# Optimization experiments

Hardware: AMD Instinct MI355X
Metric: run time of the kernel (lower is better)

## Reference

```python
import jax, jax.numpy as jnp
import numpy as np

H = 16  # hidden_dim
EPS = 1e-5


def _lstm_layer(x, W_ih, W_hh, b_ih, b_hh):
    # x: [B,T,D_in] -> [B,T,H]; PyTorch gate order i,f,g,o
    B = x.shape[0]
    xg = jnp.einsum('btd,gd->btg', x, W_ih) + (b_ih + b_hh)  # [B,T,4H]

    def step(carry, xt):
        h, c = carry
        gates = xt + h @ W_hh.T
        i, f, g, o = jnp.split(gates, 4, axis=-1)
        c = jax.nn.sigmoid(f) * c + jax.nn.sigmoid(i) * jnp.tanh(g)
        h = jax.nn.sigmoid(o) * jnp.tanh(c)
        return (h, c), h

    h0 = jnp.zeros((B, H), x.dtype)
    _, hs = jax.lax.scan(step, (h0, h0), jnp.swapaxes(xg, 0, 1))  # [T,B,H]
    return jnp.swapaxes(hs, 0, 1)


def setup_inputs() -> dict:
    key = jax.random.key(0)
    ks = jax.random.split(key, 20)
    B, T, D, O = 256, 2048, 57, 4
    x = jax.random.normal(ks[0], (B, T, D), dtype=jnp.float32)
    lengths = jnp.maximum(jnp.sort(jax.random.randint(ks[1], (B,), 1, T + 1))[::-1], 1)
    s = 1.0 / np.sqrt(H)
    u = lambda k, shp: jax.random.uniform(k, shp, jnp.float32, -s, s)
    inp = {'x': x, 'lengths': lengths}
    dims_in = [D, H, H]
    for l in range(3):
        inp[f'W_ih{l}'] = u(ks[2 + 4 * l], (4 * H, dims_in[l]))
        inp[f'W_hh{l}'] = u(ks[3 + 4 * l], (4 * H, H))
        inp[f'b_ih{l}'] = u(ks[4 + 4 * l], (4 * H,))
        inp[f'b_hh{l}'] = u(ks[5 + 4 * l], (4 * H,))
    inp['bn_gamma'] = jnp.ones((H,), jnp.float32)
    inp['bn_beta'] = jnp.zeros((H,), jnp.float32)
    inp['fc_w'] = u(ks[14], (O, H))
    inp['fc_b'] = u(ks[15], (O,))
    return inp


def reference(x, lengths, W_ih0, W_hh0, b_ih0, b_hh0, W_ih1, W_hh1, b_ih1, b_hh1,
              W_ih2, W_hh2, b_ih2, b_hh2, bn_gamma, bn_beta, fc_w, fc_b):
    B, T, _ = x.shape
    h = x
    for W_ih, W_hh, b_ih, b_hh in ((W_ih0, W_hh0, b_ih0, b_hh0),
                                    (W_ih1, W_hh1, b_ih1, b_hh1),
                                    (W_ih2, W_hh2, b_ih2, b_hh2)):
        h = _lstm_layer(h, W_ih, W_hh, b_ih, b_hh)
    # pad_packed_sequence: zero out positions past each sequence length
    mask = (jnp.arange(T)[None, :] < lengths[:, None])[:, :, None].astype(h.dtype)
    h = h * mask  # [B,T,H]
    # BatchNorm1d (training mode) over (batch,time) per channel, incl. padding zeros
    mean = jnp.mean(h, axis=(0, 1))
    var = jnp.mean((h - mean) ** 2, axis=(0, 1))
    norm = (h - mean) * jax.lax.rsqrt(var + EPS) * bn_gamma + bn_beta
    return norm @ fc_w.T + fc_b  # [B,T,4]
```

## Files before the change

kernel.cpp:

```cpp
#include <hip/hip_runtime.h>
#include <math.h>

#define TT 2048
#define BBATCH 256
#define DDIM 57
#define NROWS (BBATCH*TT)
#define NF 524288.0f
#define U 8

#define K1 (-1.4426950408889634f)
#define K2 (-2.8853900817779268f)

__device__ __forceinline__ float bcastl(float v, int k) {
  return __uint_as_float((unsigned)__builtin_amdgcn_readlane((int)__float_as_uint(v), k));
}
__device__ __forceinline__ float rcpf(float x) { return __builtin_amdgcn_rcpf(x); }
__device__ __forceinline__ float exp2f_(float x) { return __builtin_amdgcn_exp2f(x); }

template<int PAT>
__device__ __forceinline__ float quadb(float v) {
  return __int_as_float(__builtin_amdgcn_update_dpp(0, __float_as_int(v), PAT, 0xF, 0xF, true));
}

__global__ void zero_accum_k(float* accum) {
  accum[threadIdx.x] = 0.f;
}

__global__ __launch_bounds__(256) void xg0_gemm_k(
    const float* __restrict__ x, const float* __restrict__ Wih,
    const float* __restrict__ bih, const float* __restrict__ bhh,
    float* __restrict__ xg0)
{
  const int lane = threadIdx.x & 63;
  const int g = (lane & 3) * 16 + (lane >> 2);
  const float fac = ((lane & 3) == 2) ? K2 : K1;
  const int wid  = blockIdx.x * (blockDim.x >> 6) + (threadIdx.x >> 6);
  const int nw   = gridDim.x * (blockDim.x >> 6);
  float w[DDIM];
  #pragma unroll
  for (int d = 0; d < DDIM; ++d) w[d] = fac * Wih[g*DDIM + d];
  const float bias = fac * (bih[g] + bhh[g]);

  int r = wid;
  float xv = 0.f;
  if (r < NROWS && lane < DDIM)
    xv = x[(size_t)__builtin_amdgcn_readfirstlane(r) * DDIM + lane];
  for (; r < NROWS; r += nw) {
    const int rn = r + nw;
    float xn = 0.f;
    if (rn < NROWS && lane < DDIM)
      xn = x[(size_t)__builtin_amdgcn_readfirstlane(rn) * DDIM + lane];
    float a0 = bias, a1 = 0.f, a2 = 0.f, a3 = 0.f;
    #pragma unroll
    for (int d = 0; d < 56; d += 4) {
      a0 += w[d]   * bcastl(xv, d);
      a1 += w[d+1] * bcastl(xv, d+1);
      a2 += w[d+2] * bcastl(xv, d+2);
      a3 += w[d+3] * bcastl(xv, d+3);
    }
    a0 += w[56] * bcastl(xv, 56);
    xg0[(size_t)__builtin_amdgcn_readfirstlane(r) * 64 + lane] = (a0 + a1) + (a2 + a3);
    xv = xn;
  }
}

__global__ __launch_bounds__(192, 1) void lstm_scan_pipe_k(
    const float* __restrict__ xg0,
    const int*   __restrict__ lengths,
    const float* __restrict__ Whh0,
    const float* __restrict__ Wih1, const float* __restrict__ Whh1,
    const float* __restrict__ bih1, const float* __restrict__ bhh1,
    const float* __restrict__ Wih2, const float* __restrict__ Whh2,
    const float* __restrict__ bih2, const float* __restrict__ bhh2,
    float* __restrict__ h2buf, float* __restrict__ accum)
{
  const int tid  = threadIdx.x;
  const int wave = tid >> 6;
  const int lane = tid & 63;
  const int gt   = lane & 3;
  const int ch   = lane >> 2;
  const int g    = gt*16 + ch;
  const int b    = blockIdx.x;
  const int len  = lengths[b];
  const bool isg = (gt == 2);
  const float fac = isg ? K2 : K1;
  const float mg = isg ? 2.f : 1.f;
  const float ag = isg ? -1.f : 0.f;

  __shared__ float lds_h0[2][U][16];
  __shared__ float lds_h1[2][U][16];

  float wa[16], wb[16];
  float bias = 0.f;
  if (wave == 0) {
    #pragma unroll
    for (int k = 0; k < 16; ++k) { wb[k] = fac * Whh0[g*16 + k]; wa[k] = 0.f; }
  } else if (wave == 1) {
    #pragma unroll
    for (int k = 0; k < 16; ++k) { wa[k] = fac * Wih1[g*16 + k]; wb[k] = fac * Whh1[g*16 + k]; }
    bias = fac * (bih1[g] + bhh1[g]);
  } else {
    #pragma unroll
    for (int k = 0; k < 16; ++k) { wa[k] = fac * Wih2[g*16 + k]; wb[k] = fac * Whh2[g*16 + k]; }
    bias = fac * (bih2[g] + bhh2[g]);
  }

  float hs = 0.f, csK = 0.f;
  float sum = 0.f, sq = 0.f;
  const int base = b*TT*64 + lane;
  float* __restrict__ h2row = h2buf + (size_t)b*TT*16;

  auto lstm_update = [&](float dot) {
    float s   = rcpf(1.f + exp2f_(dot));
    float act = fmaf(s, mg, ag);
    float gi = quadb<0x00>(act);
    float gf = quadb<0x55>(act);
    float gg = quadb<0xAA>(act);
    float go = quadb<0xFF>(act);
    csK = fmaf(gf, csK, (K2 * gg) * gi);
    float r = rcpf(1.f + exp2f_(csK));
    hs = go * fmaf(2.f, r, -1.f);
  };
  auto owndot = [&](float seed) {
    float hb[16];
    #pragma unroll
    for (int k = 0; k < 16; ++k) hb[k] = bcastl(hs, 4*k);
    float a0 = seed, a1 = 0.f, a2 = 0.f, a3 = 0.f;
    #pragma unroll
    for (int k = 0; k < 16; k += 4) {
      a0 += wb[k]   * hb[k];
      a1 += wb[k+1] * hb[k+1];
      a2 += wb[k+2] * hb[k+2];
      a3 += wb[k+3] * hb[k+3];
    }
    return (a0 + a1) + (a2 + a3);
  };
  auto indot = [&](const float* hin) {
    float a0 = bias, a1 = 0.f, a2 = 0.f, a3 = 0.f;
    #pragma unroll
    for (int k = 0; k < 16; k += 4) {
      a0 += wa[k]   * hin[k];
      a1 += wa[k+1] * hin[k+1];
      a2 += wa[k+2] * hin[k+2];
      a3 += wa[k+3] * hin[k+3];
    }
    return (a0 + a1) + (a2 + a3);
  };

  const int NS = (len + U - 1) / U;
  const int S  = NS + 2;

  float cur[U], nxt[U];
  if (wave == 0) {
    #pragma unroll
    for (int j = 0; j < U; ++j) cur[j] = xg0[base + j*64];
    #pragma unroll
    for (int j = 0; j < U; ++j) {
      int ip = U + j; ip = ip > TT-1 ? TT-1 : ip;
      nxt[j] = xg0[base + ip*64];
    }
  }

  for (int s = 0; s < S; ++s) {
    const int p = s & 1, q = p ^ 1;
    if (wave == 0) {
      if (s < NS) {
        float ld[U];
        #pragma unroll
        for (int j = 0; j < U; ++j) {
          int ip = (s + 2)*U + j; ip = ip > TT-1 ? TT-1 : ip;
          ld[j] = xg0[base + ip*64];
        }
        #pragma unroll
        for (int j = 0; j < U; ++j) {
          lstm_update(owndot(cur[j]));
          if (gt == 0) lds_h0[p][j][ch] = hs;
        }
        #pragma unroll
        for (int j = 0; j < U; ++j) { cur[j] = nxt[j]; nxt[j] = ld[j]; }
      }
    } else if (wave == 1) {
      if (s >= 1 && s <= NS) {
        float xin[U];
        #pragma unroll
        for (int j = 0; j < U; ++j) {
          const float4* hp = (const float4*)&lds_h0[q][j][0];
          float4 h0v = hp[0], h1v = hp[1], h2v = hp[2], h3v = hp[3];
          float hin[16] = {h0v.x,h0v.y,h0v.z,h0v.w, h1v.x,h1v.y,h1v.z,h1v.w,
                           h2v.x,h2v.y,h2v.z,h2v.w, h3v.x,h3v.y,h3v.z,h3v.w};
          xin[j] = indot(hin);
        }
        #pragma unroll
        for (int j = 0; j < U; ++j) {
          lstm_update(owndot(xin[j]));
          if (gt == 0) lds_h1[p][j][ch] = hs;
        }
      }
    } else {
      if (s >= 2) {
        float xin[U];
        #pragma unroll
        for (int j = 0; j < U; ++j) {
          const float4* hp = (const float4*)&lds_h1[q][j][0];
          float4 h0v = hp[0], h1v = hp[1], h2v = hp[2], h3v = hp[3];
          float hin[16] = {h0v.x,h0v.y,h0v.z,h0v.w, h1v.x,h1v.y,h1v.z,h1v.w,
                           h2v.x,h2v.y,h2v.z,h2v.w, h3v.x,h3v.y,h3v.z,h3v.w};
          xin[j] = indot(hin);
        }
        #pragma unroll
        for (int j = 0; j < U; ++j) {
          lstm_update(owndot(xin[j]));
          const int t = (s - 2)*U + j;
          if (t < len) {
            if (gt == 0) h2row[t*16 + ch] = hs;
            sum += hs; sq += hs*hs;
          }
        }
      }
    }
    __syncthreads();
  }

  for (int idx = len*16 + tid; idx < TT*16; idx += 192)
    h2row[idx] = 0.f;

  if (wave == 2 && gt == 0) {
    atomicAdd(&accum[ch],      sum);
    atomicAdd(&accum[16 + ch], sq);
  }
}

__global__ void prep_k(const float* __restrict__ accum,
                       const float* __restrict__ gamma, const float* __restrict__ beta,
                       const float* __restrict__ fcw, const float* __restrict__ fcb,
                       float* __restrict__ coef)
{
  const int lane = threadIdx.x;
  const int o = lane >> 4, c = lane & 15;
  const float inv_n = 1.0f / NF;
  float mean = accum[c] * inv_n;
  float var  = accum[16 + c] * inv_n - mean*mean;
  float s  = gamma[c] * rsqrtf(var + 1e-5f);
  float tb = beta[c] - mean * s;
  float woc = fcw[o*16 + c];
  coef[lane] = s * woc;
  float term = tb * woc;
  #pragma unroll
  for (int off = 1; off < 16; off <<= 1) term += __shfl_xor(term, off, 16);
  if (c == 0) coef[64 + o] = fcb[o] + term;
}

__global__ __launch_bounds__(256) void finalize_k(
    const float* __restrict__ h2buf, const float* __restrict__ coef,
    float* __restrict__ out)
{
  const int r = blockIdx.x * 256 + threadIdx.x;
  const float4* hp = (const float4*)(h2buf + (size_t)r * 16);
  float4 v0 = hp[0], v1 = hp[1], v2 = hp[2], v3 = hp[3];
  float hv[16] = {v0.x,v0.y,v0.z,v0.w, v1.x,v1.y,v1.z,v1.w,
                  v2.x,v2.y,v2.z,v2.w, v3.x,v3.y,v3.z,v3.w};
  float4 o4;
  float* op = &o4.x;
  #pragma unroll
  for (int o = 0; o < 4; ++o) {
    float a = coef[64 + o];
    #pragma unroll
    for (int c = 0; c < 16; ++c) a += coef[o*16 + c] * hv[c];
    op[o] = a;
  }
  ((float4*)out)[r] = o4;
}

extern "C" void kernel_launch(void* const* d_in, const int* in_sizes, int n_in,
                              void* d_out, int out_size, void* d_ws, size_t ws_size,
                              hipStream_t stream)
{
  const float* x     = (const float*)d_in[0];
  const int* lengths = (const int*)d_in[1];
  const float* W_ih0 = (const float*)d_in[2];
  const float* W_hh0 = (const float*)d_in[3];
  const float* b_ih0 = (const float*)d_in[4];
  const float* b_hh0 = (const float*)d_in[5];
  const float* W_ih1 = (const float*)d_in[6];
  const float* W_hh1 = (const float*)d_in[7];
  const float* b_ih1 = (const float*)d_in[8];
  const float* b_hh1 = (const float*)d_in[9];
  const float* W_ih2 = (const float*)d_in[10];
  const float* W_hh2 = (const float*)d_in[11];
  const float* b_ih2 = (const float*)d_in[12];
  const float* b_hh2 = (const float*)d_in[13];
  const float* gamma = (const float*)d_in[14];
  const float* beta  = (const float*)d_in[15];
  const float* fcw   = (const float*)d_in[16];
  const float* fcb   = (const float*)d_in[17];
  float* out = (float*)d_out;

  float* ws    = (float*)d_ws;
  float* xg0   = ws;
  float* h2    = ws + 33554432;
  float* accum = ws + 33554432 + 8388608;
  float* coef  = accum + 32;

  hipLaunchKernelGGL(zero_accum_k, dim3(1), dim3(32), 0, stream, accum);
  hipLaunchKernelGGL(xg0_gemm_k, dim3(2048), dim3(256), 0, stream,
                     x, W_ih0, b_ih0, b_hh0, xg0);
  hipLaunchKernelGGL(lstm_scan_pipe_k, dim3(256), dim3(192), 0, stream,
                     xg0, lengths, W_hh0, W_ih1, W_hh1, b_ih1, b_hh1,
                     W_ih2, W_hh2, b_ih2, b_hh2, h2, accum);
  hipLaunchKernelGGL(prep_k, dim3(1), dim3(64), 0, stream,
                     accum, gamma, beta, fcw, fcb, coef);
  hipLaunchKernelGGL(finalize_k, dim3(2048), dim3(256), 0, stream, h2, coef, out);
}
```

Measured before the change: 691.3 us.

## Fuse layer-0 input projection into the LSTM scan as a fourth producer wave

Drops the separate xg0 GEMM kernel and its 128 MB intermediate buffer. A fourth wave per block now loads x rows, computes the layer-0 input projection, and hands it to wave 0 through double-buffered LDS, one chunk ahead of the scan. This removes a full-size global write and read-back of xg0. In exchange the projection work is only as parallel as the scan (256 blocks) and must keep pace with the recurrence, and the new wave adds register pressure and a fourth participant in every barrier.

After: 704.1 us. Within noise of the previous version (+1.8%).

```diff
diff --git a/kernel.cpp b/kernel.cpp
--- a/kernel.cpp
+++ b/kernel.cpp
@@ -4,7 +4,6 @@
 #define TT 2048
 #define BBATCH 256
 #define DDIM 57
-#define NROWS (BBATCH*TT)
 #define NF 524288.0f
 #define U 8
 
@@ -26,48 +25,11 @@
   accum[threadIdx.x] = 0.f;
 }
 
-__global__ __launch_bounds__(256) void xg0_gemm_k(
-    const float* __restrict__ x, const float* __restrict__ Wih,
-    const float* __restrict__ bih, const float* __restrict__ bhh,
-    float* __restrict__ xg0)
-{
-  const int lane = threadIdx.x & 63;
-  const int g = (lane & 3) * 16 + (lane >> 2);
-  const float fac = ((lane & 3) == 2) ? K2 : K1;
-  const int wid  = blockIdx.x * (blockDim.x >> 6) + (threadIdx.x >> 6);
-  const int nw   = gridDim.x * (blockDim.x >> 6);
-  float w[DDIM];
-  #pragma unroll
-  for (int d = 0; d < DDIM; ++d) w[d] = fac * Wih[g*DDIM + d];
-  const float bias = fac * (bih[g] + bhh[g]);
-
-  int r = wid;
-  float xv = 0.f;
-  if (r < NROWS && lane < DDIM)
-    xv = x[(size_t)__builtin_amdgcn_readfirstlane(r) * DDIM + lane];
-  for (; r < NROWS; r += nw) {
-    const int rn = r + nw;
-    float xn = 0.f;
-    if (rn < NROWS && lane < DDIM)
-      xn = x[(size_t)__builtin_amdgcn_readfirstlane(rn) * DDIM + lane];
-    float a0 = bias, a1 = 0.f, a2 = 0.f, a3 = 0.f;
-    #pragma unroll
-    for (int d = 0; d < 56; d += 4) {
-      a0 += w[d]   * bcastl(xv, d);
-      a1 += w[d+1] * bcastl(xv, d+1);
-      a2 += w[d+2] * bcastl(xv, d+2);
-      a3 += w[d+3] * bcastl(xv, d+3);
-    }
-    a0 += w[56] * bcastl(xv, 56);
-    xg0[(size_t)__builtin_amdgcn_readfirstlane(r) * 64 + lane] = (a0 + a1) + (a2 + a3);
-    xv = xn;
-  }
-}
-
-__global__ __launch_bounds__(192, 1) void lstm_scan_pipe_k(
-    const float* __restrict__ xg0,
+__global__ __launch_bounds__(256, 1) void lstm_fused_k(
+    const float* __restrict__ x,
     const int*   __restrict__ lengths,
-    const float* __restrict__ Whh0,
+    const float* __restrict__ Wih0, const float* __restrict__ Whh0,
+    const float* __restrict__ bih0, const float* __restrict__ bhh0,
     const float* __restrict__ Wih1, const float* __restrict__ Whh1,
     const float* __restrict__ bih1, const float* __restrict__ bhh1,
     const float* __restrict__ Wih2, const float* __restrict__ Whh2,
@@ -89,9 +51,11 @@
 
   __shared__ float lds_h0[2][U][16];
   __shared__ float lds_h1[2][U][16];
+  __shared__ float lds_xg[2][U][64];
 
   float wa[16], wb[16];
   float bias = 0.f;
+  float wx[DDIM];
   if (wave == 0) {
     #pragma unroll
     for (int k = 0; k < 16; ++k) { wb[k] = fac * Whh0[g*16 + k]; wa[k] = 0.f; }
@@ -99,16 +63,20 @@
     #pragma unroll
     for (int k = 0; k < 16; ++k) { wa[k] = fac * Wih1[g*16 + k]; wb[k] = fac * Whh1[g*16 + k]; }
     bias = fac * (bih1[g] + bhh1[g]);
-  } else {
+  } else if (wave == 2) {
     #pragma unroll
     for (int k = 0; k < 16; ++k) { wa[k] = fac * Wih2[g*16 + k]; wb[k] = fac * Whh2[g*16 + k]; }
     bias = fac * (bih2[g] + bhh2[g]);
+  } else {
+    #pragma unroll
+    for (int d = 0; d < DDIM; ++d) wx[d] = fac * Wih0[g*DDIM + d];
+    bias = fac * (bih0[g] + bhh0[g]);
   }
 
   float hs = 0.f, csK = 0.f;
   float sum = 0.f, sq = 0.f;
-  const int base = b*TT*64 + lane;
   float* __restrict__ h2row = h2buf + (size_t)b*TT*16;
+  const float* __restrict__ xseq = x + (size_t)b*TT*DDIM;
 
   auto lstm_update = [&](float dot) {
     float s   = rcpf(1.f + exp2f_(dot));
@@ -146,38 +114,54 @@
     }
     return (a0 + a1) + (a2 + a3);
   };
+  auto xgdot = [&](float xv) {
+    float xb[DDIM];
+    #pragma unroll
+    for (int d = 0; d < DDIM; ++d) xb[d] = bcastl(xv, d);
+    float a0 = bias, a1 = 0.f, a2 = 0.f, a3 = 0.f;
+    #pragma unroll
+    for (int d = 0; d < 56; d += 4) {
+      a0 += wx[d]   * xb[d];
+      a1 += wx[d+1] * xb[d+1];
+      a2 += wx[d+2] * xb[d+2];
+      a3 += wx[d+3] * xb[d+3];
+    }
+    a0 += wx[56] * xb[56];
+    return (a0 + a1) + (a2 + a3);
+  };
 
   const int NS = (len + U - 1) / U;
   const int S  = NS + 2;
 
-  float cur[U], nxt[U];
-  if (wave == 0) {
-    #pragma unroll
-    for (int j = 0; j < U; ++j) cur[j] = xg0[base + j*64];
+  float xrc[U], xrn[U];
+  if (wave == 3) {
     #pragma unroll
     for (int j = 0; j < U; ++j) {
-      int ip = U + j; ip = ip > TT-1 ? TT-1 : ip;
-      nxt[j] = xg0[base + ip*64];
-    }
-  }
+      int t = j; t = t > TT-1 ? TT-1 : t;
+      xrc[j] = (lane < DDIM) ? xseq[(size_t)t*DDIM + lane] : 0.f;
+    }
+    #pragma unroll
+    for (int j = 0; j < U; ++j) lds_xg[0][j][lane] = xgdot(xrc[j]);
+    #pragma unroll
+    for (int j = 0; j < U; ++j) {
+      int t = U + j; t = t > TT-1 ? TT-1 : t;
+      xrc[j] = (lane < DDIM) ? xseq[(size_t)t*DDIM + lane] : 0.f;
+    }
+  }
+  __syncthreads();
 
   for (int s = 0; s < S; ++s) {
     const int p = s & 1, q = p ^ 1;
     if (wave == 0) {
       if (s < NS) {
-        float ld[U];
-        #pragma unroll
-        for (int j = 0; j < U; ++j) {
-          int ip = (s + 2)*U + j; ip = ip > TT-1 ? TT-1 : ip;
-          ld[j] = xg0[base + ip*64];
-        }
-        #pragma unroll
-        for (int j = 0; j < U; ++j) {
-          lstm_update(owndot(cur[j]));
+        float xgv[U];
+        #pragma unroll
+        for (int j = 0; j < U; ++j) xgv[j] = lds_xg[p][j][lane];
+        #pragma unroll
+        for (int j = 0; j < U; ++j) {
+          lstm_update(owndot(xgv[j]));
           if (gt == 0) lds_h0[p][j][ch] = hs;
         }
-        #pragma unroll
-        for (int j = 0; j < U; ++j) { cur[j] = nxt[j]; nxt[j] = ld[j]; }
       }
     } else if (wave == 1) {
       if (s >= 1 && s <= NS) {
@@ -196,7 +180,7 @@
           if (gt == 0) lds_h1[p][j][ch] = hs;
         }
       }
-    } else {
+    } else if (wave == 2) {
       if (s >= 2) {
         float xin[U];
         #pragma unroll
@@ -217,11 +201,23 @@
           }
         }
       }
+    } else {
+      #pragma unroll
+      for (int j = 0; j < U; ++j) {
+        int t = (s + 2)*U + j; t = t > TT-1 ? TT-1 : t;
+        xrn[j] = (lane < DDIM) ? xseq[(size_t)t*DDIM + lane] : 0.f;
+      }
+      if (s + 1 < NS) {
+        #pragma unroll
+        for (int j = 0; j < U; ++j) lds_xg[q][j][lane] = xgdot(xrc[j]);
+      }
+      #pragma unroll
+      for (int j = 0; j < U; ++j) xrc[j] = xrn[j];
     }
     __syncthreads();
   }
 
-  for (int idx = len*16 + tid; idx < TT*16; idx += 192)
+  for (int idx = len*16 + tid; idx < TT*16; idx += 256)
     h2row[idx] = 0.f;
 
   if (wave == 2 && gt == 0) {
@@ -296,16 +292,14 @@
   float* out = (float*)d_out;
 
   float* ws    = (float*)d_ws;
-  float* xg0   = ws;
-  float* h2    = ws + 33554432;
-  float* accum = ws + 33554432 + 8388608;
+  float* h2    = ws;
+  float* accum = ws + 8388608;
   float* coef  = accum + 32;
 
   hipLaunchKernelGGL(zero_accum_k, dim3(1), dim3(32), 0, stream, accum);
-  hipLaunchKernelGGL(xg0_gemm_k, dim3(2048), dim3(256), 0, stream,
-                     x, W_ih0, b_ih0, b_hh0, xg0);
-  hipLaunchKernelGGL(lstm_scan_pipe_k, dim3(256), dim3(192), 0, stream,
-                     xg0, lengths, W_hh0, W_ih1, W_hh1, b_ih1, b_hh1,
+  hipLaunchKernelGGL(lstm_fused_k, dim3(256), dim3(256), 0, stream,
+                     x, lengths, W_ih0, W_hh0, b_ih0, b_hh0,
+                     W_ih1, W_hh1, b_ih1, b_hh1,
                      W_ih2, W_hh2, b_ih2, b_hh2, h2, accum);
   hipLaunchKernelGGL(prep_k, dim3(1), dim3(64), 0, stream,
                      accum, gamma, beta, fcw, fcb, coef);
```
